# Kernel tuning notes

Hardware: AMD Instinct MI355X
Metric: run time of the kernel (lower is better)

Reference implementation:

```python
import jax, jax.numpy as jnp
import numpy as np

D_MODEL = 1024
N_EXPERTS = 8
TOP_K = 2
D_FF = 4 * D_MODEL
BATCH, SEQ = 4, 2048


def setup_inputs() -> dict:
    key = jax.random.key(0)
    k0, k1, k2, k3 = jax.random.split(key, 4)
    scale = 0.02
    x = jax.random.normal(k0, (BATCH, SEQ, D_MODEL), dtype=jnp.float32)
    # gate: nn.Linear(d_model, num_experts, bias=False) -> x @ Wg
    Wg = (jax.random.normal(k1, (D_MODEL, N_EXPERTS), dtype=jnp.float32) * scale)
    # stacked expert weights: W1[e]: d_model->4*d_model, W2[e]: 4*d_model->d_model
    W1 = (jax.random.normal(k2, (N_EXPERTS, D_MODEL, D_FF), dtype=jnp.float32) * scale)
    W2 = (jax.random.normal(k3, (N_EXPERTS, D_FF, D_MODEL), dtype=jnp.float32) * scale)
    return {"x": x, "Wg": Wg, "W1": W1, "W2": W2}


def reference(x, Wg, W1, W2):
    B, S, D = x.shape
    xf = x.reshape(-1, D)                      # [T, D], T = B*S
    gate_logits = xf @ Wg                      # [T, E]
    gate_probs = jax.nn.softmax(gate_logits, axis=-1)
    top_v, top_i = jax.lax.top_k(gate_probs, TOP_K)   # [T, K]
    top_v = top_v / (top_v.sum(axis=-1, keepdims=True) + 1e-8)
    # combine weights per (token, expert): 0 for unselected experts, so the
    # dense-weighted sum below equals the original gather/MLP/scatter loop.
    comb = jnp.sum(jax.nn.one_hot(top_i, N_EXPERTS, dtype=gate_probs.dtype)
                   * top_v[..., None], axis=1)        # [T, E]
    out = jnp.zeros_like(xf)
    for e in range(N_EXPERTS):                 # fixed small expert loop
        h = jax.nn.gelu(xf @ W1[e], approximate=False)   # exact GELU, as torch default
        out = out + comb[:, e:e + 1] * (h @ W2[e])
    # load-balance loss
    router_probs = gate_probs.mean(axis=0)             # [E]
    usage = jnp.sum(jax.nn.one_hot(top_i.reshape(-1), N_EXPERTS,
                                   dtype=gate_probs.dtype), axis=0)
    usage = usage / usage.sum()
    load_balance_loss = N_EXPERTS * jnp.sum(router_probs * usage)
    return out.reshape(B, S, D), load_balance_loss
```

## Files before the change

kernel.cpp:

```cpp
#include <hip/hip_runtime.h>
#include <math.h>
#include <stdint.h>

#define TOKENS 8192
#define DMODEL 1024
#define DFF    4096
#define NEXP   8
#define NROWS  (TOKENS * 2)

typedef float          vf4 __attribute__((ext_vector_type(4)));
typedef unsigned short vu4 __attribute__((ext_vector_type(4)));
typedef short          vs8 __attribute__((ext_vector_type(8)));
typedef float          facc __attribute__((ext_vector_type(4)));

__device__ __forceinline__ unsigned short f2bf(float f) {
    union { float f; unsigned u; } v; v.f = f;
    return (unsigned short)((v.u + 0x7FFFu + ((v.u >> 16) & 1u)) >> 16);
}
__device__ __forceinline__ int imin(int a, int b) { return a < b ? a : b; }

__device__ __forceinline__ void gl2lds16(const void* g, void* l) {
    __builtin_amdgcn_global_load_lds(
        (const __attribute__((address_space(1))) unsigned int*)g,
        (__attribute__((address_space(3))) unsigned int*)l, 16, 0, 0);
}

__global__ void k_convert_x(const float* __restrict__ x, unsigned short* __restrict__ xbf) {
    int i = blockIdx.x * 256 + threadIdx.x;
    vf4 v = ((const vf4*)x)[i];
    vu4 o;
    o[0] = f2bf(v[0]); o[1] = f2bf(v[1]); o[2] = f2bf(v[2]); o[3] = f2bf(v[3]);
    ((vu4*)xbf)[i] = o;
}

__global__ void k_transpose_bf(const float* __restrict__ src, unsigned short* __restrict__ dst,
                               int R, int C) {
    __shared__ float tile[64][65];
    const int e = blockIdx.z;
    const float* s = src + (size_t)e * R * C;
    unsigned short* d = dst + (size_t)e * R * C;
    const int r0 = blockIdx.y * 64, c0 = blockIdx.x * 64;
    const int tr = threadIdx.x >> 4;
    const int tc = (threadIdx.x & 15) * 4;
    #pragma unroll
    for (int p = 0; p < 4; ++p) {
        int r = p * 16 + tr;
        vf4 v = *(const vf4*)(s + (size_t)(r0 + r) * C + c0 + tc);
        tile[r][tc + 0] = v[0]; tile[r][tc + 1] = v[1];
        tile[r][tc + 2] = v[2]; tile[r][tc + 3] = v[3];
    }
    __syncthreads();
    #pragma unroll
    for (int p = 0; p < 4; ++p) {
        int cc = p * 16 + tr;
        vu4 o;
        o[0] = f2bf(tile[tc + 0][cc]); o[1] = f2bf(tile[tc + 1][cc]);
        o[2] = f2bf(tile[tc + 2][cc]); o[3] = f2bf(tile[tc + 3][cc]);
        *(vu4*)(d + (size_t)(c0 + cc) * R + r0 + tc) = o;
    }
}

__global__ void k_gate(const float* __restrict__ x, const float* __restrict__ Wg,
                       float* __restrict__ probs,
                       int* __restrict__ tk_e, float* __restrict__ tk_w) {
    const int t = blockIdx.x;
    const int lane = threadIdx.x;
    float acc[NEXP] = {0.f, 0.f, 0.f, 0.f, 0.f, 0.f, 0.f, 0.f};
    const float* xr = x + (size_t)t * DMODEL;
    #pragma unroll
    for (int i = 0; i < 16; ++i) {
        int dd = i * 64 + lane;
        float xv = xr[dd];
        const vf4* w = (const vf4*)(Wg + (size_t)dd * NEXP);
        vf4 a = w[0], b = w[1];
        acc[0] += xv * a[0]; acc[1] += xv * a[1]; acc[2] += xv * a[2]; acc[3] += xv * a[3];
        acc[4] += xv * b[0]; acc[5] += xv * b[1]; acc[6] += xv * b[2]; acc[7] += xv * b[3];
    }
    #pragma unroll
    for (int e = 0; e < NEXP; ++e) {
        float v = acc[e];
        for (int off = 32; off; off >>= 1) v += __shfl_xor(v, off, 64);
        acc[e] = v;
    }
    if (lane == 0) {
        float mx = acc[0];
        #pragma unroll
        for (int e = 1; e < NEXP; ++e) mx = fmaxf(mx, acc[e]);
        float p[NEXP], s = 0.f;
        #pragma unroll
        for (int e = 0; e < NEXP; ++e) { p[e] = expf(acc[e] - mx); s += p[e]; }
        float inv = 1.f / s;
        #pragma unroll
        for (int e = 0; e < NEXP; ++e) p[e] *= inv;
        vf4 p0 = {p[0], p[1], p[2], p[3]}, p1 = {p[4], p[5], p[6], p[7]};
        ((vf4*)(probs + (size_t)t * NEXP))[0] = p0;
        ((vf4*)(probs + (size_t)t * NEXP))[1] = p1;
        int i0 = 0; float b0 = p[0];
        #pragma unroll
        for (int e = 1; e < NEXP; ++e) if (p[e] > b0) { b0 = p[e]; i0 = e; }
        int i1 = -1; float b1 = -1.f;
        #pragma unroll
        for (int e = 0; e < NEXP; ++e) if (e != i0 && p[e] > b1) { b1 = p[e]; i1 = e; }
        float sn = 1.f / (b0 + b1 + 1e-8f);
        tk_e[t * 2 + 0] = i0; tk_w[t * 2 + 0] = b0 * sn;
        tk_e[t * 2 + 1] = i1; tk_w[t * 2 + 1] = b1 * sn;
    }
}

__global__ void k_reduce(const float* __restrict__ probs, const int* __restrict__ tk_e,
                         float* __restrict__ probsum, int* __restrict__ counts) {
    __shared__ float psum_l[4][NEXP];
    __shared__ int hist_l[NEXP];
    const int tid = threadIdx.x;
    const int wave = tid >> 6, lane = tid & 63;
    const int t = blockIdx.x * 256 + tid;
    if (tid < NEXP) hist_l[tid] = 0;
    vf4 p0 = ((const vf4*)(probs + (size_t)t * NEXP))[0];
    vf4 p1 = ((const vf4*)(probs + (size_t)t * NEXP))[1];
    float p[NEXP] = {p0[0], p0[1], p0[2], p0[3], p1[0], p1[1], p1[2], p1[3]};
    #pragma unroll
    for (int e = 0; e < NEXP; ++e) {
        float v = p[e];
        for (int off = 32; off; off >>= 1) v += __shfl_xor(v, off, 64);
        p[e] = v;
    }
    if (lane == 0) {
        #pragma unroll
        for (int e = 0; e < NEXP; ++e) psum_l[wave][e] = p[e];
    }
    __syncthreads();
    atomicAdd(&hist_l[tk_e[t * 2 + 0]], 1);
    atomicAdd(&hist_l[tk_e[t * 2 + 1]], 1);
    __syncthreads();
    if (tid < NEXP) {
        float s = psum_l[0][tid] + psum_l[1][tid] + psum_l[2][tid] + psum_l[3][tid];
        atomicAdd(&probsum[tid], s);
        atomicAdd(&counts[tid], hist_l[tid]);
    }
}

__global__ void k_finalize(const int* __restrict__ counts, const float* __restrict__ probsum,
                           int* __restrict__ bases, float* __restrict__ out_loss) {
    if (threadIdx.x == 0) {
        int b = 0; float loss = 0.f;
        for (int e = 0; e < NEXP; ++e) {
            bases[e] = b; b += counts[e];
            loss += (probsum[e] / (float)TOKENS) * ((float)counts[e] / (float)NROWS);
        }
        out_loss[0] = (float)NEXP * loss;
    }
}

__global__ void k_build(const int* __restrict__ tk_e, const float* __restrict__ tk_w,
                        const int* __restrict__ bases, int* __restrict__ cursors,
                        int* __restrict__ row_token, float* __restrict__ row_weight) {
    __shared__ int hist_l[NEXP];
    __shared__ int base_l[NEXP];
    const int tid = threadIdx.x;
    const int i = blockIdx.x * 256 + tid;
    if (tid < NEXP) hist_l[tid] = 0;
    __syncthreads();
    const int e = tk_e[i];
    const int rank = atomicAdd(&hist_l[e], 1);
    __syncthreads();
    if (tid < NEXP) base_l[tid] = atomicAdd(&cursors[tid], hist_l[tid]);
    __syncthreads();
    const int row = bases[e] + base_l[e] + rank;
    row_token[row] = i >> 1;
    row_weight[row] = tk_w[i];
}

__global__ __launch_bounds__(256) void k_ffn1(
    const unsigned short* __restrict__ xbf, const unsigned short* __restrict__ w1t,
    const int* __restrict__ counts, const int* __restrict__ bases,
    const int* __restrict__ row_token, unsigned short* __restrict__ h) {
    __shared__ unsigned short As[128 * 32];
    __shared__ unsigned short Bs[128 * 32];
    const int e = blockIdx.z;
    const int cnt = counts[e];
    const int m0 = blockIdx.y * 128;
    if (m0 >= cnt) return;
    const int n0 = blockIdx.x * 128;
    const int rb = bases[e];
    const int tid = threadIdx.x;
    const int wave = tid >> 6, lane = tid & 63;

    const int rA0 = tid >> 2,        pA0 = tid & 3;
    const int rA1 = (256 + tid) >> 2, pA1 = tid & 3;
    const int t0 = row_token[rb + imin(m0 + rA0, cnt - 1)];
    const int t1 = row_token[rb + imin(m0 + rA1, cnt - 1)];
    const unsigned short* gA0 = xbf + (size_t)t0 * DMODEL + pA0 * 8;
    const unsigned short* gA1 = xbf + (size_t)t1 * DMODEL + pA1 * 8;
    const unsigned short* gB0 = w1t + ((size_t)e * DFF + n0 + rA0) * DMODEL + pA0 * 8;
    const unsigned short* gB1 = w1t + ((size_t)e * DFF + n0 + rA1) * DMODEL + pA1 * 8;
    unsigned short* lA0 = As + (size_t)(wave * 64) * 8;
    unsigned short* lA1 = As + (size_t)(256 + wave * 64) * 8;
    unsigned short* lB0 = Bs + (size_t)(wave * 64) * 8;
    unsigned short* lB1 = Bs + (size_t)(256 + wave * 64) * 8;

    const int wm = (wave >> 1) * 64, wn = (wave & 1) * 64;
    const int mrow = lane & 15, kq = (lane >> 4) * 8;
    facc acc[4][4] = {};

    for (int kb = 0; kb < DMODEL; kb += 32) {
        gl2lds16(gA0 + kb, lA0);
        gl2lds16(gA1 + kb, lA1);
        gl2lds16(gB0 + kb, lB0);
        gl2lds16(gB1 + kb, lB1);
        __syncthreads();
        vs8 af[4], bfr[4];
        #pragma unroll
        for (int i = 0; i < 4; ++i)
            af[i] = *(const vs8*)(As + (wm + i * 16 + mrow) * 32 + kq);
        #pragma unroll
        for (int i = 0; i < 4; ++i)
            bfr[i] = *(const vs8*)(Bs + (wn + i * 16 + mrow) * 32 + kq);
        #pragma unroll
        for (int i = 0; i < 4; ++i)
            #pragma unroll
            for (int j = 0; j < 4; ++j)
                acc[i][j] = __builtin_amdgcn_mfma_f32_16x16x32_bf16(af[i], bfr[j], acc[i][j], 0, 0, 0);
        __syncthreads();
    }

    const int quad = lane >> 4, col = lane & 15;
    #pragma unroll
    for (int i = 0; i < 4; ++i) {
        #pragma unroll
        for (int r = 0; r < 4; ++r) {
            const int mloc = wm + i * 16 + quad * 4 + r;
            if (m0 + mloc < cnt) {
                unsigned short* hrow = h + (size_t)(rb + m0 + mloc) * DFF + n0;
                #pragma unroll
                for (int j = 0; j < 4; ++j) {
                    float v = acc[i][j][r];
                    v = 0.5f * v * (1.0f + erff(v * 0.70710678118654752f));
                    hrow[wn + j * 16 + col] = f2bf(v);
                }
            }
        }
    }
}

__global__ __launch_bounds__(256) void k_ffn2(
    const unsigned short* __restrict__ h, const unsigned short* __restrict__ w2t,
    const int* __restrict__ counts, const int* __restrict__ bases,
    const int* __restrict__ row_token, const float* __restrict__ row_weight,
    float* __restrict__ out) {
    __shared__ unsigned short As[128 * 32];
    __shared__ unsigned short Bs[128 * 32];
    __shared__ int   tokl[128];
    __shared__ float wl[128];
    const int e = blockIdx.z;
    const int cnt = counts[e];
    const int m0 = blockIdx.y * 128;
    if (m0 >= cnt) return;
    const int n0 = blockIdx.x * 128;
    const int rb = bases[e];
    const int tid = threadIdx.x;
    const int wave = tid >> 6, lane = tid & 63;

    if (tid < 128) {
        int gr = m0 + tid;
        bool vv = gr < cnt;
        tokl[tid] = vv ? row_token[rb + gr] : 0;
        wl[tid]   = vv ? row_weight[rb + gr] : 0.0f;
    }

    const int rA0 = tid >> 2,         pA0 = tid & 3;
    const int rA1 = (256 + tid) >> 2, pA1 = tid & 3;
    const unsigned short* gA0 = h + (size_t)(rb + imin(m0 + rA0, cnt - 1)) * DFF + pA0 * 8;
    const unsigned short* gA1 = h + (size_t)(rb + imin(m0 + rA1, cnt - 1)) * DFF + pA1 * 8;
    const unsigned short* gB0 = w2t + ((size_t)e * DMODEL + n0 + rA0) * DFF + pA0 * 8;
    const unsigned short* gB1 = w2t + ((size_t)e * DMODEL + n0 + rA1) * DFF + pA1 * 8;
    unsigned short* lA0 = As + (size_t)(wave * 64) * 8;
    unsigned short* lA1 = As + (size_t)(256 + wave * 64) * 8;
    unsigned short* lB0 = Bs + (size_t)(wave * 64) * 8;
    unsigned short* lB1 = Bs + (size_t)(256 + wave * 64) * 8;

    const int wm = (wave >> 1) * 64, wn = (wave & 1) * 64;
    const int mrow = lane & 15, kq = (lane >> 4) * 8;
    facc acc[4][4] = {};

    for (int kb = 0; kb < DFF; kb += 32) {
        gl2lds16(gA0 + kb, lA0);
        gl2lds16(gA1 + kb, lA1);
        gl2lds16(gB0 + kb, lB0);
        gl2lds16(gB1 + kb, lB1);
        __syncthreads();
        vs8 af[4], bfr[4];
        #pragma unroll
        for (int i = 0; i < 4; ++i)
            af[i] = *(const vs8*)(As + (wm + i * 16 + mrow) * 32 + kq);
        #pragma unroll
        for (int i = 0; i < 4; ++i)
            bfr[i] = *(const vs8*)(Bs + (wn + i * 16 + mrow) * 32 + kq);
        #pragma unroll
        for (int i = 0; i < 4; ++i)
            #pragma unroll
            for (int j = 0; j < 4; ++j)
                acc[i][j] = __builtin_amdgcn_mfma_f32_16x16x32_bf16(af[i], bfr[j], acc[i][j], 0, 0, 0);
        __syncthreads();
    }

    const int quad = lane >> 4, col = lane & 15;
    #pragma unroll
    for (int i = 0; i < 4; ++i) {
        #pragma unroll
        for (int r = 0; r < 4; ++r) {
            const int mloc = wm + i * 16 + quad * 4 + r;
            if (m0 + mloc < cnt) {
                const float w = wl[mloc];
                float* orow = out + (size_t)tokl[mloc] * DMODEL + n0;
                #pragma unroll
                for (int j = 0; j < 4; ++j)
                    atomicAdd(&orow[wn + j * 16 + col], acc[i][j][r] * w);
            }
        }
    }
}

extern "C" void kernel_launch(void* const* d_in, const int* in_sizes, int n_in,
                              void* d_out, int out_size, void* d_ws, size_t ws_size,
                              hipStream_t stream) {
    const float* x  = (const float*)d_in[0];
    const float* Wg = (const float*)d_in[1];
    const float* W1 = (const float*)d_in[2];
    const float* W2 = (const float*)d_in[3];
    float* out = (float*)d_out;

    char* ws = (char*)d_ws;
    int*   counts     = (int*)  (ws + 0);
    int*   cursors    = (int*)  (ws + 32);
    float* probsum    = (float*)(ws + 64);
    int*   bases      = (int*)  (ws + 96);
    int*   tk_e       = (int*)  (ws + 256);
    float* tk_w       = (float*)(ws + 256 + 65536);
    int*   row_token  = (int*)  (ws + 256 + 131072);
    float* row_weight = (float*)(ws + 256 + 196608);
    float* probs      = (float*)(ws + 262400);
    unsigned short* xbf = (unsigned short*)(ws + 524544);
    unsigned short* w1t = xbf + (size_t)TOKENS * DMODEL;
    unsigned short* w2t = w1t + (size_t)NEXP * DMODEL * DFF;
    unsigned short* hbuf = w2t + (size_t)NEXP * DMODEL * DFF;

    hipMemsetAsync(d_out, 0, (size_t)out_size * sizeof(float), stream);
    hipMemsetAsync(ws, 0, 256, stream);

    k_convert_x<<<(TOKENS * DMODEL) / 1024, 256, 0, stream>>>(x, xbf);
    k_transpose_bf<<<dim3(DFF / 64, DMODEL / 64, NEXP), 256, 0, stream>>>(W1, w1t, DMODEL, DFF);
    k_transpose_bf<<<dim3(DMODEL / 64, DFF / 64, NEXP), 256, 0, stream>>>(W2, w2t, DFF, DMODEL);
    k_gate<<<TOKENS, 64, 0, stream>>>(x, Wg, probs, tk_e, tk_w);
    k_reduce<<<TOKENS / 256, 256, 0, stream>>>(probs, tk_e, probsum, counts);
    k_finalize<<<1, 64, 0, stream>>>(counts, probsum, bases, out + (out_size - 1));
    k_build<<<NROWS / 256, 256, 0, stream>>>(tk_e, tk_w, bases, cursors, row_token, row_weight);
    k_ffn1<<<dim3(DFF / 128, TOKENS / 128, NEXP), 256, 0, stream>>>(xbf, w1t, counts, bases, row_token, hbuf);
    k_ffn2<<<dim3(DMODEL / 128, TOKENS / 128, NEXP), 256, 0, stream>>>(hbuf, w2t, counts, bases, row_token, row_weight, out);
}
```

Measured before the change: 835.4 us.

## Widen GEMM K-tile to 64 with XOR-swizzled LDS and XCD-aware block remap

The expert FFN GEMMs now load a K depth of 64 per iteration, which halves the barrier count, and they store tiles in LDS with a rotating 16-byte chunk swizzle to avoid bank conflicts on fragment reads. The 3D grid is flattened into a 1D grid. Block indices are remapped so that consecutive blocks, which land on different XCDs, share M/N tile clusters for better L2 reuse. The gate kernel also packs four tokens per 256-thread block. LDS use per block doubles, which may reduce occupancy.

```diff
diff --git a/kernel.cpp b/kernel.cpp
--- a/kernel.cpp
+++ b/kernel.cpp
@@ -63,8 +63,8 @@
 __global__ void k_gate(const float* __restrict__ x, const float* __restrict__ Wg,
                        float* __restrict__ probs,
                        int* __restrict__ tk_e, float* __restrict__ tk_w) {
-    const int t = blockIdx.x;
-    const int lane = threadIdx.x;
+    const int wave = threadIdx.x >> 6, lane = threadIdx.x & 63;
+    const int t = blockIdx.x * 4 + wave;
     float acc[NEXP] = {0.f, 0.f, 0.f, 0.f, 0.f, 0.f, 0.f, 0.f};
     const float* xr = x + (size_t)t * DMODEL;
     #pragma unroll
@@ -174,52 +174,65 @@
     const unsigned short* __restrict__ xbf, const unsigned short* __restrict__ w1t,
     const int* __restrict__ counts, const int* __restrict__ bases,
     const int* __restrict__ row_token, unsigned short* __restrict__ h) {
-    __shared__ unsigned short As[128 * 32];
-    __shared__ unsigned short Bs[128 * 32];
-    const int e = blockIdx.z;
+    __shared__ unsigned short As[128 * 64];
+    __shared__ unsigned short Bs[128 * 64];
+    const int L = blockIdx.x;
+    const int c = L & 7, j = L >> 3;
+    const int e = j >> 8;
+    const int r = j & 255;
+    const int n_in = r & 1, m_in = (r >> 1) & 3;
+    const int cl = ((r >> 3) << 3) | c;
+    const int m_cl = cl & 15, n_cl = cl >> 4;
+    const int n0 = (n_cl * 2 + n_in) * 128;
+    const int m0 = (m_cl * 4 + m_in) * 128;
     const int cnt = counts[e];
-    const int m0 = blockIdx.y * 128;
     if (m0 >= cnt) return;
-    const int n0 = blockIdx.x * 128;
     const int rb = bases[e];
     const int tid = threadIdx.x;
     const int wave = tid >> 6, lane = tid & 63;
 
-    const int rA0 = tid >> 2,        pA0 = tid & 3;
-    const int rA1 = (256 + tid) >> 2, pA1 = tid & 3;
-    const int t0 = row_token[rb + imin(m0 + rA0, cnt - 1)];
-    const int t1 = row_token[rb + imin(m0 + rA1, cnt - 1)];
-    const unsigned short* gA0 = xbf + (size_t)t0 * DMODEL + pA0 * 8;
-    const unsigned short* gA1 = xbf + (size_t)t1 * DMODEL + pA1 * 8;
-    const unsigned short* gB0 = w1t + ((size_t)e * DFF + n0 + rA0) * DMODEL + pA0 * 8;
-    const unsigned short* gB1 = w1t + ((size_t)e * DFF + n0 + rA1) * DMODEL + pA1 * 8;
-    unsigned short* lA0 = As + (size_t)(wave * 64) * 8;
-    unsigned short* lA1 = As + (size_t)(256 + wave * 64) * 8;
-    unsigned short* lB0 = Bs + (size_t)(wave * 64) * 8;
-    unsigned short* lB1 = Bs + (size_t)(256 + wave * 64) * 8;
+    const unsigned short* gA[4];
+    const unsigned short* gB[4];
+    #pragma unroll
+    for (int i = 0; i < 4; ++i) {
+        const int s = i * 256 + tid;
+        const int row = s >> 3, q = s & 7, p = (q - row) & 7;
+        const int t = row_token[rb + imin(m0 + row, cnt - 1)];
+        gA[i] = xbf + (size_t)t * DMODEL + p * 8;
+        gB[i] = w1t + ((size_t)e * DFF + n0 + row) * DMODEL + p * 8;
+    }
 
     const int wm = (wave >> 1) * 64, wn = (wave & 1) * 64;
-    const int mrow = lane & 15, kq = (lane >> 4) * 8;
+    const int mrow = lane & 15, g = lane >> 4;
     facc acc[4][4] = {};
 
-    for (int kb = 0; kb < DMODEL; kb += 32) {
-        gl2lds16(gA0 + kb, lA0);
-        gl2lds16(gA1 + kb, lA1);
-        gl2lds16(gB0 + kb, lB0);
-        gl2lds16(gB1 + kb, lB1);
+    for (int kb = 0; kb < DMODEL; kb += 64) {
+        #pragma unroll
+        for (int i = 0; i < 4; ++i) {
+            gl2lds16(gA[i] + kb, As + (i * 256 + tid) * 8);
+            gl2lds16(gB[i] + kb, Bs + (i * 256 + tid) * 8);
+        }
         __syncthreads();
-        vs8 af[4], bfr[4];
-        #pragma unroll
-        for (int i = 0; i < 4; ++i)
-            af[i] = *(const vs8*)(As + (wm + i * 16 + mrow) * 32 + kq);
-        #pragma unroll
-        for (int i = 0; i < 4; ++i)
-            bfr[i] = *(const vs8*)(Bs + (wn + i * 16 + mrow) * 32 + kq);
-        #pragma unroll
-        for (int i = 0; i < 4; ++i)
-            #pragma unroll
-            for (int j = 0; j < 4; ++j)
-                acc[i][j] = __builtin_amdgcn_mfma_f32_16x16x32_bf16(af[i], bfr[j], acc[i][j], 0, 0, 0);
+        #pragma unroll
+        for (int ks = 0; ks < 2; ++ks) {
+            const int pa = ks * 4 + g;
+            vs8 af[4], bfr[4];
+            #pragma unroll
+            for (int i = 0; i < 4; ++i) {
+                const int rowa = wm + i * 16 + mrow;
+                af[i] = *(const vs8*)(As + rowa * 64 + ((pa + rowa) & 7) * 8);
+            }
+            #pragma unroll
+            for (int jj = 0; jj < 4; ++jj) {
+                const int rowb = wn + jj * 16 + mrow;
+                bfr[jj] = *(const vs8*)(Bs + rowb * 64 + ((pa + rowb) & 7) * 8);
+            }
+            #pragma unroll
+            for (int i = 0; i < 4; ++i)
+                #pragma unroll
+                for (int jj = 0; jj < 4; ++jj)
+                    acc[i][jj] = __builtin_amdgcn_mfma_f32_16x16x32_bf16(af[i], bfr[jj], acc[i][jj], 0, 0, 0);
+        }
         __syncthreads();
     }
 
@@ -227,15 +240,15 @@
     #pragma unroll
     for (int i = 0; i < 4; ++i) {
         #pragma unroll
-        for (int r = 0; r < 4; ++r) {
-            const int mloc = wm + i * 16 + quad * 4 + r;
+        for (int rr = 0; rr < 4; ++rr) {
+            const int mloc = wm + i * 16 + quad * 4 + rr;
             if (m0 + mloc < cnt) {
                 unsigned short* hrow = h + (size_t)(rb + m0 + mloc) * DFF + n0;
                 #pragma unroll
-                for (int j = 0; j < 4; ++j) {
-                    float v = acc[i][j][r];
+                for (int jj = 0; jj < 4; ++jj) {
+                    float v = acc[i][jj][rr];
                     v = 0.5f * v * (1.0f + erff(v * 0.70710678118654752f));
-                    hrow[wn + j * 16 + col] = f2bf(v);
+                    hrow[wn + jj * 16 + col] = f2bf(v);
                 }
             }
         }
@@ -247,15 +260,21 @@
     const int* __restrict__ counts, const int* __restrict__ bases,
     const int* __restrict__ row_token, const float* __restrict__ row_weight,
     float* __restrict__ out) {
-    __shared__ unsigned short As[128 * 32];
-    __shared__ unsigned short Bs[128 * 32];
+    __shared__ unsigned short As[128 * 64];
+    __shared__ unsigned short Bs[128 * 64];
     __shared__ int   tokl[128];
     __shared__ float wl[128];
-    const int e = blockIdx.z;
+    const int L = blockIdx.x;
+    const int c = L & 7, j = L >> 3;
+    const int e = j >> 6;
+    const int r = j & 63;
+    const int n_in = r & 1, m_in = (r >> 1) & 3;
+    const int cl = ((r >> 3) << 3) | c;
+    const int m_cl = cl & 15, n_cl = cl >> 4;
+    const int n0 = (n_cl * 2 + n_in) * 128;
+    const int m0 = (m_cl * 4 + m_in) * 128;
     const int cnt = counts[e];
-    const int m0 = blockIdx.y * 128;
     if (m0 >= cnt) return;
-    const int n0 = blockIdx.x * 128;
     const int rb = bases[e];
     const int tid = threadIdx.x;
     const int wave = tid >> 6, lane = tid & 63;
@@ -267,39 +286,47 @@
         wl[tid]   = vv ? row_weight[rb + gr] : 0.0f;
     }
 
-    const int rA0 = tid >> 2,         pA0 = tid & 3;
-    const int rA1 = (256 + tid) >> 2, pA1 = tid & 3;
-    const unsigned short* gA0 = h + (size_t)(rb + imin(m0 + rA0, cnt - 1)) * DFF + pA0 * 8;
-    const unsigned short* gA1 = h + (size_t)(rb + imin(m0 + rA1, cnt - 1)) * DFF + pA1 * 8;
-    const unsigned short* gB0 = w2t + ((size_t)e * DMODEL + n0 + rA0) * DFF + pA0 * 8;
-    const unsigned short* gB1 = w2t + ((size_t)e * DMODEL + n0 + rA1) * DFF + pA1 * 8;
-    unsigned short* lA0 = As + (size_t)(wave * 64) * 8;
-    unsigned short* lA1 = As + (size_t)(256 + wave * 64) * 8;
-    unsigned short* lB0 = Bs + (size_t)(wave * 64) * 8;
-    unsigned short* lB1 = Bs + (size_t)(256 + wave * 64) * 8;
+    const unsigned short* gA[4];
+    const unsigned short* gB[4];
+    #pragma unroll
+    for (int i = 0; i < 4; ++i) {
+        const int s = i * 256 + tid;
+        const int row = s >> 3, q = s & 7, p = (q - row) & 7;
+        gA[i] = h + (size_t)(rb + imin(m0 + row, cnt - 1)) * DFF + p * 8;
+        gB[i] = w2t + ((size_t)e * DMODEL + n0 + row) * DFF + p * 8;
+    }
 
     const int wm = (wave >> 1) * 64, wn = (wave & 1) * 64;
-    const int mrow = lane & 15, kq = (lane >> 4) * 8;
+    const int mrow = lane & 15, g = lane >> 4;
     facc acc[4][4] = {};
 
-    for (int kb = 0; kb < DFF; kb += 32) {
-        gl2lds16(gA0 + kb, lA0);
-        gl2lds16(gA1 + kb, lA1);
-        gl2lds16(gB0 + kb, lB0);
-        gl2lds16(gB1 + kb, lB1);
+    for (int kb = 0; kb < DFF; kb += 64) {
+        #pragma unroll
+        for (int i = 0; i < 4; ++i) {
+            gl2lds16(gA[i] + kb, As + (i * 256 + tid) * 8);
+            gl2lds16(gB[i] + kb, Bs + (i * 256 + tid) * 8);
+        }
         __syncthreads();
-        vs8 af[4], bfr[4];
-        #pragma unroll
-        for (int i = 0; i < 4; ++i)
-            af[i] = *(const vs8*)(As + (wm + i * 16 + mrow) * 32 + kq);
-        #pragma unroll
-        for (int i = 0; i < 4; ++i)
-            bfr[i] = *(const vs8*)(Bs + (wn + i * 16 + mrow) * 32 + kq);
-        #pragma unroll
-        for (int i = 0; i < 4; ++i)
-            #pragma unroll
-            for (int j = 0; j < 4; ++j)
-                acc[i][j] = __builtin_amdgcn_mfma_f32_16x16x32_bf16(af[i], bfr[j], acc[i][j], 0, 0, 0);
+        #pragma unroll
+        for (int ks = 0; ks < 2; ++ks) {
+            const int pa = ks * 4 + g;
+            vs8 af[4], bfr[4];
+            #pragma unroll
+            for (int i = 0; i < 4; ++i) {
+                const int rowa = wm + i * 16 + mrow;
+                af[i] = *(const vs8*)(As + rowa * 64 + ((pa + rowa) & 7) * 8);
+            }
+            #pragma unroll
+            for (int jj = 0; jj < 4; ++jj) {
+                const int rowb = wn + jj * 16 + mrow;
+                bfr[jj] = *(const vs8*)(Bs + rowb * 64 + ((pa + rowb) & 7) * 8);
+            }
+            #pragma unroll
+            for (int i = 0; i < 4; ++i)
+                #pragma unroll
+                for (int jj = 0; jj < 4; ++jj)
+                    acc[i][jj] = __builtin_amdgcn_mfma_f32_16x16x32_bf16(af[i], bfr[jj], acc[i][jj], 0, 0, 0);
+        }
         __syncthreads();
     }
 
@@ -307,14 +334,14 @@
     #pragma unroll
     for (int i = 0; i < 4; ++i) {
         #pragma unroll
-        for (int r = 0; r < 4; ++r) {
-            const int mloc = wm + i * 16 + quad * 4 + r;
+        for (int rr = 0; rr < 4; ++rr) {
+            const int mloc = wm + i * 16 + quad * 4 + rr;
             if (m0 + mloc < cnt) {
                 const float w = wl[mloc];
                 float* orow = out + (size_t)tokl[mloc] * DMODEL + n0;
                 #pragma unroll
-                for (int j = 0; j < 4; ++j)
-                    atomicAdd(&orow[wn + j * 16 + col], acc[i][j][r] * w);
+                for (int jj = 0; jj < 4; ++jj)
+                    atomicAdd(&orow[wn + jj * 16 + col], acc[i][jj][rr] * w);
             }
         }
     }
@@ -350,10 +377,10 @@
     k_convert_x<<<(TOKENS * DMODEL) / 1024, 256, 0, stream>>>(x, xbf);
     k_transpose_bf<<<dim3(DFF / 64, DMODEL / 64, NEXP), 256, 0, stream>>>(W1, w1t, DMODEL, DFF);
     k_transpose_bf<<<dim3(DMODEL / 64, DFF / 64, NEXP), 256, 0, stream>>>(W2, w2t, DFF, DMODEL);
-    k_gate<<<TOKENS, 64, 0, stream>>>(x, Wg, probs, tk_e, tk_w);
+    k_gate<<<TOKENS / 4, 256, 0, stream>>>(x, Wg, probs, tk_e, tk_w);
     k_reduce<<<TOKENS / 256, 256, 0, stream>>>(probs, tk_e, probsum, counts);
     k_finalize<<<1, 64, 0, stream>>>(counts, probsum, bases, out + (out_size - 1));
     k_build<<<NROWS / 256, 256, 0, stream>>>(tk_e, tk_w, bases, cursors, row_token, row_weight);
-    k_ffn1<<<dim3(DFF / 128, TOKENS / 128, NEXP), 256, 0, stream>>>(xbf, w1t, counts, bases, row_token, hbuf);
-    k_ffn2<<<dim3(DMODEL / 128, TOKENS / 128, NEXP), 256, 0, stream>>>(hbuf, w2t, counts, bases, row_token, row_weight, out);
-}
+    k_ffn1<<<16384, 256, 0, stream>>>(xbf, w1t, counts, bases, row_token, hbuf);
+    k_ffn2<<<4096, 256, 0, stream>>>(hbuf, w2t, counts, bases, row_token, row_weight, out);
+}
```

Measured after the change: 1.161 ms. 1.39x slower.
